# Kernel tuning notes

Hardware: AMD Instinct MI355X
Metric: run time of the kernel (lower is better)

## Reference

```python
import jax, jax.numpy as jnp
import numpy as np

B_SZ, T, C_DIM, N = 16, 2048, 128, 64
STEP = 0.01
LN_EPS = 1e-5


def _cplx(re, im):
    return (re + 1j * im).astype(jnp.complex64)


def s4_kernel(L_real, L_imag, P_real, P_imag, B_real, B_imag, C_real, C_imag, L):
    """DPLR generating-function kernel (annotated-S4 kernel_DPLR), vectorized over channels.
    Returns real kernel of shape (L, C)."""
    Lam = _cplx(jnp.minimum(L_real, 1e-4), L_imag)          # (C, N)
    P = _cplx(P_real, P_imag)                                # (C, N)
    Bm = _cplx(B_real, B_imag)                               # (C, N)
    Cm = _cplx(C_real, C_imag)                               # (C, N)
    Omega = jnp.exp(-2j * jnp.pi * jnp.arange(L) / L).astype(jnp.complex64)  # (L,)
    g = (2.0 / STEP) * ((1.0 - Omega) / (1.0 + Omega))       # (L,)
    c2 = 2.0 / (1.0 + Omega)                                 # (L,)

    def cauchy(v):  # v: (C, N) -> (L, C)
        return (v[None, :, :] / (g[:, None, None] - Lam[None, :, :])).sum(-1)

    k00 = cauchy(jnp.conj(Cm) * Bm)
    k01 = cauchy(jnp.conj(Cm) * P)
    k10 = cauchy(jnp.conj(P) * Bm)
    k11 = cauchy(jnp.conj(P) * P)
    at_roots = c2[:, None] * (k00 - k01 * (1.0 / (1.0 + k11)) * k10)  # (L, C)
    return jnp.fft.ifft(at_roots, n=L, axis=0).real          # (L, C)


def setup_inputs() -> dict:
    key = jax.random.key(0)
    ks = jax.random.split(key, 12)
    s = 1.0 / np.sqrt(N)
    return {
        "x": jax.random.normal(ks[0], (B_SZ, T, C_DIM), jnp.float32),
        "ln_gamma": jnp.ones((C_DIM,), jnp.float32),
        "ln_beta": jnp.zeros((C_DIM,), jnp.float32),
        "L_real": -0.5 * jnp.abs(jax.random.normal(ks[1], (C_DIM, N), jnp.float32)),
        "L_imag": jax.random.normal(ks[2], (C_DIM, N), jnp.float32) * float(np.pi),
        "P_real": jax.random.normal(ks[3], (C_DIM, N), jnp.float32) * s,
        "P_imag": jax.random.normal(ks[4], (C_DIM, N), jnp.float32) * s,
        "B_real": jax.random.normal(ks[5], (C_DIM, N), jnp.float32) * s,
        "B_imag": jax.random.normal(ks[6], (C_DIM, N), jnp.float32) * s,
        "C_real": jax.random.normal(ks[7], (C_DIM, N), jnp.float32) * float(np.sqrt(0.5)),
        "C_imag": jax.random.normal(ks[8], (C_DIM, N), jnp.float32) * float(np.sqrt(0.5)),
        "D": jnp.ones((C_DIM,), jnp.float32),
        "W_out": jax.random.normal(ks[9], (C_DIM, C_DIM), jnp.float32) / float(np.sqrt(C_DIM)),
        "b_out": jnp.zeros((C_DIM,), jnp.float32),
    }


def reference(x, ln_gamma, ln_beta, L_real, L_imag, P_real, P_imag,
              B_real, B_imag, C_real, C_imag, D, W_out, b_out):
    # pre-LayerNorm over channels
    mu = x.mean(-1, keepdims=True)
    var = ((x - mu) ** 2).mean(-1, keepdims=True)
    y = (x - mu) / jnp.sqrt(var + LN_EPS) * ln_gamma + ln_beta   # (B, T, C)

    # S4 FFT convolution (training path)
    kernel = s4_kernel(L_real, L_imag, P_real, P_imag,
                       B_real, B_imag, C_real, C_imag, T)       # (T, C)
    kf = jnp.fft.rfft(kernel, n=2 * T, axis=0)                  # (T+1, C)
    uf = jnp.fft.rfft(y, n=2 * T, axis=1)                        # (B, T+1, C)
    conv = jnp.fft.irfft(uf * kf[None], n=2 * T, axis=1)[:, :T, :]
    ssm_out = conv + D * y                                       # skip D*u

    # GELU (exact) -> Linear -> residual
    h = jax.nn.gelu(ssm_out, approximate=False)
    out = jnp.einsum("btc,oc->bto", h, W_out) + b_out
    return out + x
```

## Files before the change

kernel.cpp:

```cpp
#include <hip/hip_runtime.h>


#define PAD(i) ((i) + ((i) >> 4))

using bf16x8 = __attribute__((ext_vector_type(8))) short;
using f32x4 = __attribute__((ext_vector_type(4))) float;
typedef unsigned short ushort_t;

static __device__ __forceinline__ float2 cmulf(float2 a, float2 b) {
  return make_float2(a.x * b.x - a.y * b.y, a.x * b.y + a.y * b.x);
}
static __device__ __forceinline__ float2 cadd(float2 a, float2 b) { return make_float2(a.x + b.x, a.y + b.y); }
static __device__ __forceinline__ float2 csub(float2 a, float2 b) { return make_float2(a.x - b.x, a.y - b.y); }
static __device__ __forceinline__ float2 cconj(float2 a) { return make_float2(a.x, -a.y); }
static __device__ __forceinline__ float gelu1(float x) {
  float x2 = x * x;
  float z = x * fmaf(0.0356774081f, x2, 0.7978845608f);
  z = fminf(fmaxf(z, -15.0f), 15.0f);
  float e = __builtin_amdgcn_exp2f(z * 2.8853900817779268f);
  return x * e * __builtin_amdgcn_rcpf(e + 1.0f);
}
static __device__ __forceinline__ ushort_t f2bf(float f) {
  unsigned int u = __float_as_uint(f);
  u += 0x7FFFu + ((u >> 16) & 1u);
  return (ushort_t)(u >> 16);
}
static __device__ __forceinline__ float bf2f(ushort_t u) {
  return __uint_as_float(((unsigned int)u) << 16);
}
static __device__ __forceinline__ float2 twf(float rev) {
  return make_float2(__builtin_amdgcn_cosf(rev), -__builtin_amdgcn_sinf(rev));
}
static __device__ __forceinline__ float2 twi(float rev) {
  return make_float2(__builtin_amdgcn_cosf(rev), __builtin_amdgcn_sinf(rev));
}

template <bool INV>
static __device__ __forceinline__ void bf4g(float2& a, float2& b, float2& c, float2& d, float2 w1) {
  float2 t0 = cadd(a, c), t1 = csub(a, c), t2 = cadd(b, d), t3 = csub(b, d);
  float2 w2 = cmulf(w1, w1), w3 = cmulf(w2, w1);
  float2 o0 = cadd(t0, t2);
  float2 o1 = cmulf(csub(t0, t2), w2);
  float2 o2, o3;
  if (!INV) {
    o2 = cmulf(make_float2(t1.x + t3.y, t1.y - t3.x), w1);
    o3 = cmulf(make_float2(t1.x - t3.y, t1.y + t3.x), w3);
  } else {
    o2 = cmulf(make_float2(t1.x - t3.y, t1.y + t3.x), w1);
    o3 = cmulf(make_float2(t1.x + t3.y, t1.y - t3.x), w3);
  }
  a = o0; b = o1; c = o2; d = o3;
}
static __device__ __forceinline__ void bf4f(float2& a, float2& b, float2& c, float2& d, float2 w1) {
  bf4g<false>(a, b, c, d, w1);
}
static __device__ __forceinline__ void bf4f3(float2& a, float2& b, float2& c, float2& d,
                                             float2 w1, float2 w2, float2 w3) {
  float2 t0 = cadd(a, c), t1 = csub(a, c), t2 = cadd(b, d), t3 = csub(b, d);
  a = cadd(t0, t2);
  b = cmulf(csub(t0, t2), w2);
  c = cmulf(make_float2(t1.x + t3.y, t1.y - t3.x), w1);
  d = cmulf(make_float2(t1.x - t3.y, t1.y + t3.x), w3);
}
static __device__ __forceinline__ void bf4f1(float2& a, float2& b, float2& c, float2& d) {
  float2 t0 = cadd(a, c), t1 = csub(a, c), t2 = cadd(b, d), t3 = csub(b, d);
  a = cadd(t0, t2);
  b = csub(t0, t2);
  c = make_float2(t1.x + t3.y, t1.y - t3.x);
  d = make_float2(t1.x - t3.y, t1.y + t3.x);
}
static __device__ __forceinline__ void bf4f_z(float2 a, float2 b, float2 w1,
                                              float2& o0, float2& o1, float2& o2, float2& o3) {
  float2 w2 = cmulf(w1, w1), w3 = cmulf(w2, w1);
  o0 = cadd(a, b);
  o1 = cmulf(csub(a, b), w2);
  o2 = cmulf(make_float2(a.x + b.y, a.y - b.x), w1);
  o3 = cmulf(make_float2(a.x - b.y, a.y + b.x), w3);
}
template <bool INV>
static __device__ __forceinline__ void bf4h(float2& a, float2& b, float2& c, float2& d, float2 u1) {
  float2 u2 = cmulf(u1, u1);
  float2 tb = cmulf(b, u2), td = cmulf(d, u2);
  float2 a1 = cadd(a, tb), b1 = csub(a, tb), c1 = cadd(c, td), d1 = csub(c, td);
  float2 tc = cmulf(c1, u1), te = cmulf(d1, u1);
  a = cadd(a1, tc);
  c = csub(a1, tc);
  if (INV) {
    b = make_float2(b1.x - te.y, b1.y + te.x);
    d = make_float2(b1.x + te.y, b1.y - te.x);
  } else {
    b = make_float2(b1.x + te.y, b1.y - te.x);
    d = make_float2(b1.x - te.y, b1.y + te.x);
  }
}
static __device__ __forceinline__ void bf4i(float2& a, float2& b, float2& c, float2& d, float2 u1) {
  bf4h<true>(a, b, c, d, u1);
}
static __device__ __forceinline__ void bf4i3(float2& a, float2& b, float2& c, float2& d,
                                             float2 u1, float2 u2) {
  float2 tb = cmulf(b, u2), td = cmulf(d, u2);
  float2 a1 = cadd(a, tb), b1 = csub(a, tb), c1 = cadd(c, td), d1 = csub(c, td);
  float2 tc = cmulf(c1, u1), te = cmulf(d1, u1);
  a = cadd(a1, tc);
  c = csub(a1, tc);
  b = make_float2(b1.x - te.y, b1.y + te.x);
  d = make_float2(b1.x + te.y, b1.y - te.x);
}
static __device__ __forceinline__ void bf4i1(float2& a, float2& b, float2& c, float2& d) {
  float2 a1 = cadd(a, b), b1 = csub(a, b), c1 = cadd(c, d), d1 = csub(c, d);
  a = cadd(a1, c1);
  c = csub(a1, c1);
  b = make_float2(b1.x - d1.y, b1.y + d1.x);
  d = make_float2(b1.x + d1.y, b1.y - d1.x);
}

#define W256R 0.9238795325112867f
#define W256I -0.3826834323650898f
#define W512R 0.7071067811865476f
#define W512I -0.7071067811865476f
#define W768R 0.3826834323650898f
#define W768I -0.9238795325112867f

__global__ __launch_bounds__(256) void k_ln_ar(
    const float* __restrict__ x, const float* __restrict__ gamma, const float* __restrict__ beta,
    ushort_t* __restrict__ y_bf,
    const float* __restrict__ Lr, const float* __restrict__ Li,
    const float* __restrict__ Pr, const float* __restrict__ Pi,
    const float* __restrict__ Br, const float* __restrict__ Bi,
    const float* __restrict__ Cr, const float* __restrict__ Ci,
    float2* __restrict__ arr,
    const float* __restrict__ W, ushort_t* __restrict__ w_bf) {
  __shared__ __align__(16) char sm[17536];
  const int tid = threadIdx.x;
  if (blockIdx.x < 1024) {
    float* tile = (float*)sm;
    float* sg = (float*)(sm + 16512);
    float* sb = (float*)(sm + 17024);
    const int b = blockIdx.x >> 6;
    const int t0 = (blockIdx.x & 63) << 5;
    if (tid < 128) { sg[tid] = gamma[tid]; sb[tid] = beta[tid]; }
    const float4* __restrict__ xb4 = (const float4*)(x + ((size_t)b * 2048 + t0) * 128);
#pragma unroll
    for (int r = 0; r < 4; ++r) {
      int idx = tid + 256 * r;
      int t = idx >> 5, j = idx & 31;
      float4 v4 = xb4[idx];
      float* dst = &tile[t * 129 + 4 * j];
      dst[0] = v4.x; dst[1] = v4.y; dst[2] = v4.z; dst[3] = v4.w;
    }
    __syncthreads();
    const int row = tid >> 3, sgp = tid & 7;
    float sum = 0.f, sq = 0.f;
#pragma unroll
    for (int i = 0; i < 16; ++i) {
      float v = tile[row * 129 + sgp * 16 + i];
      sum += v;
      sq += v * v;
    }
    sum += __shfl_xor(sum, 1); sq += __shfl_xor(sq, 1);
    sum += __shfl_xor(sum, 2); sq += __shfl_xor(sq, 2);
    sum += __shfl_xor(sum, 4); sq += __shfl_xor(sq, 4);
    float mean = sum * (1.0f / 128.0f);
    float var = sq * (1.0f / 128.0f) - mean * mean;
    float rstd = 1.0f / sqrtf(var + 1e-5f);
#pragma unroll
    for (int i = 0; i < 16; ++i) {
      int cc = sgp * 16 + i;
      float v = tile[row * 129 + cc];
      tile[row * 129 + cc] = (v - mean) * rstd * sg[cc] + sb[cc];
    }
    __syncthreads();
    ushort_t* __restrict__ yb = y_bf + (size_t)b * 128 * 2048 + t0;
#pragma unroll
    for (int r = 0; r < 4; ++r) {
      int idx = tid + 256 * r;
      int cc = idx >> 3, tl4 = (idx & 7) * 4;
      ushort4 o4;
      o4.x = f2bf(tile[(tl4 + 0) * 129 + cc]);
      o4.y = f2bf(tile[(tl4 + 1) * 129 + cc]);
      o4.z = f2bf(tile[(tl4 + 2) * 129 + cc]);
      o4.w = f2bf(tile[(tl4 + 3) * 129 + cc]);
      *(ushort4*)(yb + (size_t)cc * 2048 + tl4) = o4;
    }
  } else if (blockIdx.x < 2048) {
    float2* sLam = (float2*)sm;
    float2* sv00 = sLam + 64;
    float2* sv01 = sLam + 128;
    float2* sv10 = sLam + 192;
    float2* sv11 = sLam + 256;
    const int id = blockIdx.x - 1024;
    const int c = id >> 3;
    const int l = ((id & 7) << 8) + tid;
    if (tid < 64) {
      int i = c * 64 + tid;
      float lr = fminf(Lr[i], 1e-4f), li = Li[i];
      float pr = Pr[i], pi = Pi[i];
      float br = Br[i], bi = Bi[i];
      float cr = Cr[i], ci = Ci[i];
      sLam[tid] = make_float2(lr, li);
      sv00[tid] = make_float2(cr * br + ci * bi, cr * bi - ci * br);
      sv01[tid] = make_float2(cr * pr + ci * pi, cr * pi - ci * pr);
      sv10[tid] = make_float2(pr * br + pi * bi, pr * bi - pi * br);
      sv11[tid] = make_float2(pr * pr + pi * pi, 0.0f);
    }
    __syncthreads();
    float theta = (-6.2831855f * (float)l) * (1.0f / 2048.0f);
    float om_i, om_r;
    sincosf(theta, &om_i, &om_r);
    float pr_ = 1.0f + om_r, pi_ = om_i;
    float mr_ = 1.0f - om_r, mi_ = -om_i;
    float invd = __builtin_amdgcn_rcpf(fmaf(pr_, pr_, pi_ * pi_));
    float gr = 200.0f * ((mr_ * pr_ + mi_ * pi_) * invd);
    float gi = 200.0f * ((mi_ * pr_ - mr_ * pi_) * invd);
    float c2r = 2.0f * pr_ * invd, c2i = -2.0f * pi_ * invd;
    float s00r = 0.f, s00i = 0.f, s01r = 0.f, s01i = 0.f;
    float s10r = 0.f, s10i = 0.f, s11r = 0.f, s11i = 0.f;
#pragma unroll 8
    for (int n = 0; n < 64; ++n) {
      float2 lam = sLam[n];
      float dr = gr - lam.x, di = gi - lam.y;
      float idn = __builtin_amdgcn_rcpf(fmaf(dr, dr, di * di));
      float ir = dr * idn, ii = -di * idn;
      float2 v;
      v = sv00[n]; s00r += v.x * ir - v.y * ii; s00i += v.x * ii + v.y * ir;
      v = sv01[n]; s01r += v.x * ir - v.y * ii; s01i += v.x * ii + v.y * ir;
      v = sv10[n]; s10r += v.x * ir - v.y * ii; s10i += v.x * ii + v.y * ir;
      v = sv11[n]; s11r += v.x * ir - v.y * ii; s11i += v.x * ii + v.y * ir;
    }
    float dr2 = 1.0f + s11r, di2 = s11i;
    float idn2 = __builtin_amdgcn_rcpf(fmaf(dr2, dr2, di2 * di2));
    float rr = dr2 * idn2, ri = -di2 * idn2;
    float t1r = s01r * rr - s01i * ri, t1i = s01r * ri + s01i * rr;
    float t2r = t1r * s10r - t1i * s10i, t2i = t1r * s10i + t1i * s10r;
    float fr = s00r - t2r, fi = s00i - t2i;
    arr[(size_t)c * 2048 + l] = make_float2(c2r * fr - c2i * fi, c2r * fi + c2i * fr);
  } else {
    const float4* __restrict__ W4 = (const float4*)W;
    ushort4* __restrict__ Wb4 = (ushort4*)w_bf;
#pragma unroll
    for (int m = 0; m < 16; ++m) {
      int idx = tid + 256 * m;
      float4 w4 = W4[idx];
      ushort4 u;
      u.x = f2bf(w4.x); u.y = f2bf(w4.y); u.z = f2bf(w4.z); u.w = f2bf(w4.w);
      Wb4[idx] = u;
    }
  }
}

template <int Q, bool INV>
static __device__ __forceinline__ void kfs_dif(float2* s, int tid) {
  constexpr float SCR = (float)(2048 / (4 * Q)) * (1.0f / 2048.0f);
  int k = tid;
  int j = k & (Q - 1);
  int i = ((k - j) << 2) + j;
  float2 w1 = INV ? twi((float)j * SCR) : twf((float)j * SCR);
  float2 a = s[PAD(i)], b = s[PAD(i + Q)], c2 = s[PAD(i + 2 * Q)], d = s[PAD(i + 3 * Q)];
  bf4g<INV>(a, b, c2, d, w1);
  s[PAD(i)] = a; s[PAD(i + Q)] = b; s[PAD(i + 2 * Q)] = c2; s[PAD(i + 3 * Q)] = d;
  __syncthreads();
}
template <int Q>
static __device__ __forceinline__ void kfs_dit(float2* s, int tid) {
  constexpr float SCR = (float)(2048 / (4 * Q)) * (1.0f / 2048.0f);
  int k = tid;
  int j = k & (Q - 1);
  int i = ((k - j) << 2) + j;
  float2 u1 = twf((float)j * SCR);
  float2 a = s[PAD(i)], b = s[PAD(i + Q)], c2 = s[PAD(i + 2 * Q)], d = s[PAD(i + 3 * Q)];
  bf4h<false>(a, b, c2, d, u1);
  s[PAD(i)] = a; s[PAD(i + Q)] = b; s[PAD(i + 2 * Q)] = c2; s[PAD(i + 3 * Q)] = d;
  __syncthreads();
}
static __device__ __forceinline__ void kfs_r2(float2* s, int tid) {
#pragma unroll
  for (int m = 0; m < 2; ++m) {
    int k = tid + 512 * m;
    int i = 2 * k;
    float2 a = s[PAD(i)], b = s[PAD(i + 1)];
    s[PAD(i)] = cadd(a, b);
    s[PAD(i + 1)] = csub(a, b);
  }
  __syncthreads();
}

__global__ __launch_bounds__(512) void k_kf(const float2* __restrict__ arr, float2* __restrict__ kf) {
  __shared__ float2 s[2176];
  const int tid = threadIdx.x;
  const int c = blockIdx.x;
  const float2* __restrict__ ac = arr + (size_t)c * 2048;
  float2* __restrict__ kfc = kf + (size_t)c * 4096;
#pragma unroll
  for (int m = 0; m < 4; ++m) {
    int q = tid + 512 * m;
    float2 aq = ac[q];
    s[PAD(q)] = aq;
    float2 am = ac[(2048 - q) & 2047];
    kfc[__brev((unsigned)q) >> 21] =
        make_float2((aq.x + am.x) * (0.5f / 4096.0f), (aq.y - am.y) * (0.5f / 4096.0f));
  }
  __syncthreads();
  kfs_dif<512, true>(s, tid);
  kfs_dif<128, true>(s, tid);
  kfs_dif<32, true>(s, tid);
  kfs_dif<8, true>(s, tid);
  kfs_dif<2, true>(s, tid);
  kfs_r2(s, tid);
#pragma unroll
  for (int m = 0; m < 4; ++m) {
    int p = tid + 512 * m;
    int t = (int)(__brev((unsigned)p) >> 21);
    float2 w = twf((float)t * (1.0f / 4096.0f));
    float kr = s[PAD(p)].x * (1.0f / 8388608.0f);
    s[PAD(p)] = make_float2(kr * w.x, kr * w.y);
  }
  __syncthreads();
  kfs_r2(s, tid);
  kfs_dit<2>(s, tid);
  kfs_dit<8>(s, tid);
  kfs_dit<32>(s, tid);
  kfs_dit<128>(s, tid);
  kfs_dit<512>(s, tid);
#pragma unroll
  for (int m = 0; m < 4; ++m) {
    int q = tid + 512 * m;
    kfc[2048 + (int)(__brev((unsigned)q) >> 21)] = s[PAD(q)];
  }
}

__global__ __launch_bounds__(256) void k_conv(const ushort_t* __restrict__ y_bf,
                                              const float2* __restrict__ kf,
                                              const float* __restrict__ D,
                                              ushort_t* __restrict__ h_bf) {
  __shared__ float2 s[4352];
  const int tid = threadIdx.x;
  const int p = blockIdx.x;
  const int b = p >> 7, c = p & 127;
  const ushort_t* __restrict__ r1 = y_bf + (size_t)(b * 128 + c) * 2048;
  const ushort_t* __restrict__ r2 = y_bf + (size_t)((b + 8) * 128 + c) * 2048;
  ushort_t* __restrict__ hb1 = h_bf + (size_t)(b * 128 + c) * 2048;
  ushort_t* __restrict__ hb2 = h_bf + (size_t)((b + 8) * 128 + c) * 2048;

  const float2 K1 = make_float2(W256R, W256I);
  const float2 K2 = make_float2(W512R, W512I);
  const float2 K3 = make_float2(W768R, W768I);

  float2 kreg[16];
  {
    const float2* __restrict__ kfc = kf + (size_t)c * 4096 + 16 * tid;
#pragma unroll
    for (int e = 0; e < 16; ++e) kreg[e] = kfc[e];
  }
  const float Dc = D[c];

  float2 v[16];
  {
    float2 ya[8];
#pragma unroll
    for (int e = 0; e < 8; ++e)
      ya[e] = make_float2(bf2f(r1[tid + 256 * e]), bf2f(r2[tid + 256 * e]));
    const float2 wt = twf((float)tid * (1.0f / 4096.0f));
    bf4f_z(ya[0], ya[4], wt,            v[0], v[4], v[8], v[12]);
    bf4f_z(ya[1], ya[5], cmulf(wt, K1), v[1], v[5], v[9], v[13]);
    bf4f_z(ya[2], ya[6], cmulf(wt, K2), v[2], v[6], v[10], v[14]);
    bf4f_z(ya[3], ya[7], cmulf(wt, K3), v[3], v[7], v[11], v[15]);
  }
  {
    const float2 wq = twf((float)tid * (1.0f / 1024.0f));
    const float2 wq2 = cmulf(wq, wq), wq3 = cmulf(wq2, wq);
    bf4f3(v[0], v[1], v[2], v[3], wq, wq2, wq3);
    bf4f3(v[4], v[5], v[6], v[7], wq, wq2, wq3);
    bf4f3(v[8], v[9], v[10], v[11], wq, wq2, wq3);
    bf4f3(v[12], v[13], v[14], v[15], wq, wq2, wq3);
  }
  {
    const int wb0 = tid + (tid >> 4);
#pragma unroll
    for (int e = 0; e < 16; ++e) s[272 * e + wb0] = v[e];
  }
  __syncthreads();
  const int a_ = tid >> 4, b_ = tid & 15;
  const int rbB = 272 * a_ + b_;
#pragma unroll
  for (int e = 0; e < 16; ++e) v[e] = s[rbB + 17 * e];
  {
    const float2 wb = twf((float)b_ * (1.0f / 256.0f));
    bf4f(v[0], v[4], v[8], v[12], wb);
    bf4f(v[1], v[5], v[9], v[13], cmulf(wb, K1));
    bf4f(v[2], v[6], v[10], v[14], cmulf(wb, K2));
    bf4f(v[3], v[7], v[11], v[15], cmulf(wb, K3));
  }
  {
    const float2 w16 = twf((float)b_ * (1.0f / 64.0f));
    const float2 w162 = cmulf(w16, w16), w163 = cmulf(w162, w16);
    bf4f3(v[0], v[1], v[2], v[3], w16, w162, w163);
    bf4f3(v[4], v[5], v[6], v[7], w16, w162, w163);
    bf4f3(v[8], v[9], v[10], v[11], w16, w162, w163);
    bf4f3(v[12], v[13], v[14], v[15], w16, w162, w163);
  }
#pragma unroll
  for (int e = 0; e < 16; ++e) s[rbB + 17 * e] = v[e];
  __syncthreads();
#pragma unroll
  for (int e = 0; e < 16; ++e) v[e] = s[17 * tid + e];
  __builtin_amdgcn_s_setprio(1);
  bf4f1(v[0], v[4], v[8], v[12]);
  bf4f(v[1], v[5], v[9], v[13], K1);
  bf4f(v[2], v[6], v[10], v[14], K2);
  bf4f(v[3], v[7], v[11], v[15], K3);
  bf4f1(v[0], v[1], v[2], v[3]);
  bf4f1(v[4], v[5], v[6], v[7]);
  bf4f1(v[8], v[9], v[10], v[11]);
  bf4f1(v[12], v[13], v[14], v[15]);
  {
    const float dsc = Dc * (1.0f / 4096.0f);
#pragma unroll
    for (int e = 0; e < 16; ++e) {
      float2 kv = kreg[e];
      kv.x += dsc;
      v[e] = cmulf(v[e], kv);
    }
  }
  bf4i1(v[0], v[1], v[2], v[3]);
  bf4i1(v[4], v[5], v[6], v[7]);
  bf4i1(v[8], v[9], v[10], v[11]);
  bf4i1(v[12], v[13], v[14], v[15]);
  bf4i1(v[0], v[4], v[8], v[12]);
  bf4i(v[1], v[5], v[9], v[13], cconj(K1));
  bf4i(v[2], v[6], v[10], v[14], cconj(K2));
  bf4i(v[3], v[7], v[11], v[15], cconj(K3));
  __builtin_amdgcn_s_setprio(0);
#pragma unroll
  for (int e = 0; e < 16; ++e) s[17 * tid + e] = v[e];
  __syncthreads();
#pragma unroll
  for (int e = 0; e < 16; ++e) v[e] = s[rbB + 17 * e];
  {
    const float2 w16c = twi((float)b_ * (1.0f / 64.0f));
    const float2 w16c2 = cmulf(w16c, w16c);
    bf4i3(v[0], v[1], v[2], v[3], w16c, w16c2);
    bf4i3(v[4], v[5], v[6], v[7], w16c, w16c2);
    bf4i3(v[8], v[9], v[10], v[11], w16c, w16c2);
    bf4i3(v[12], v[13], v[14], v[15], w16c, w16c2);
  }
  {
    const float2 wbc = twi((float)b_ * (1.0f / 256.0f));
    bf4i(v[0], v[4], v[8], v[12], wbc);
    bf4i(v[1], v[5], v[9], v[13], cmulf(wbc, cconj(K1)));
    bf4i(v[2], v[6], v[10], v[14], cmulf(wbc, cconj(K2)));
    bf4i(v[3], v[7], v[11], v[15], cmulf(wbc, cconj(K3)));
  }
#pragma unroll
  for (int e = 0; e < 16; ++e) s[rbB + 17 * e] = v[e];
  __syncthreads();
  {
    const int wb0 = tid + (tid >> 4);
#pragma unroll
    for (int e = 0; e < 16; ++e) v[e] = s[272 * e + wb0];
  }
  {
    const float2 wqc = twi((float)tid * (1.0f / 1024.0f));
    const float2 wqc2 = cmulf(wqc, wqc);
    bf4i3(v[0], v[1], v[2], v[3], wqc, wqc2);
    bf4i3(v[4], v[5], v[6], v[7], wqc, wqc2);
    bf4i3(v[8], v[9], v[10], v[11], wqc, wqc2);
    bf4i3(v[12], v[13], v[14], v[15], wqc, wqc2);
  }
  const float2 wtc = twi((float)tid * (1.0f / 4096.0f));
  auto fin = [&](float2 va, float2 vb, float2 vc2, float2 vd, float2 u1, int e0) {
    float2 u2 = cmulf(u1, u1);
    float2 tb = cmulf(vb, u2), td = cmulf(vd, u2);
    float2 a1 = cadd(va, tb), b1 = csub(va, tb), c1 = cadd(vc2, td), d1 = csub(vc2, td);
    float2 tc = cmulf(c1, u1), te = cmulf(d1, u1);
    float2 oa = cadd(a1, tc);
    float2 ob = make_float2(b1.x - te.y, b1.y + te.x);
    int i0 = tid + 256 * e0;
    hb1[i0] = f2bf(gelu1(oa.x));
    hb2[i0] = f2bf(gelu1(oa.y));
    hb1[i0 + 1024] = f2bf(gelu1(ob.x));
    hb2[i0 + 1024] = f2bf(gelu1(ob.y));
  };
  fin(v[0], v[4], v[8], v[12], wtc, 0);
  fin(v[1], v[5], v[9], v[13], cmulf(wtc, cconj(K1)), 1);
  fin(v[2], v[6], v[10], v[14], cmulf(wtc, cconj(K2)), 2);
  fin(v[3], v[7], v[11], v[15], cmulf(wtc, cconj(K3)), 3);
}

__global__ __launch_bounds__(256) void k_out(const ushort_t* __restrict__ h_bf,
                                             const ushort_t* __restrict__ w_bf,
                                             const float* __restrict__ bout,
                                             const float* __restrict__ x,
                                             float* __restrict__ out) {
  __shared__ __align__(16) char smem[52224];
  ushort_t* Wl = (ushort_t*)smem;
  ushort_t* hl = (ushort_t*)(smem + 34816);
  const int tid = threadIdx.x;
  const int b = blockIdx.x >> 5;
  const int t0 = (blockIdx.x & 31) << 6;

  {
    const ushort4* __restrict__ Wb4 = (const ushort4*)w_bf;
#pragma unroll
    for (int r = 0; r < 16; ++r) {
      int idx = tid + 256 * r;
      int o = idx >> 5, j = idx & 31;
      ushort4 u = Wb4[o * 32 + j];
      int sc = (((j >> 1) ^ (o & 15)) << 3) + 4 * (j & 1);
      *(ushort4*)&Wl[o * 136 + sc] = u;
    }
  }
  {
#pragma unroll
    for (int r = 0; r < 8; ++r) {
      int idx = tid + 256 * r;
      int cc = idx >> 4, t4 = (idx & 15) * 4;
      ushort4 hv = *(const ushort4*)&h_bf[((size_t)(b * 128 + cc)) * 2048 + t0 + t4];
      int cb = cc >> 3, clo = cc & 7;
#pragma unroll
      for (int i = 0; i < 4; ++i) {
        int t = t4 + i;
        hl[t * 136 + (((cb ^ (t & 15)) << 3) + clo)] = ((const ushort_t*)&hv)[i];
      }
    }
  }
  __syncthreads();

  const int l = tid & 63;
  const int w = tid >> 6;
  const int tl = l & 15;
  const int g = l >> 4;
  f32x4 acc[8];
#pragma unroll
  for (int i = 0; i < 8; ++i) acc[i] = (f32x4){0.f, 0.f, 0.f, 0.f};

#pragma unroll
  for (int ks = 0; ks < 4; ++ks) {
    int cb = ks * 4 + g;
    int col = ((cb ^ tl) << 3);
    bf16x8 bfrag = *(const bf16x8*)&hl[(16 * w + tl) * 136 + col];
#pragma unroll
    for (int ot = 0; ot < 8; ++ot) {
      bf16x8 afrag = *(const bf16x8*)&Wl[(ot * 16 + tl) * 136 + col];
      acc[ot] = __builtin_amdgcn_mfma_f32_16x16x32_bf16(afrag, bfrag, acc[ot], 0, 0, 0);
    }
  }
  const int t = t0 + 16 * w + tl;
  const size_t rowoff = ((size_t)b * 2048 + t) * 128;
#pragma unroll
  for (int ot = 0; ot < 8; ++ot) {
    int o = ot * 16 + g * 4;
    float4 xv = *(const float4*)&x[rowoff + o];
    float4 bo4 = *(const float4*)&bout[o];
    float4 v;
    v.x = acc[ot][0] + bo4.x + xv.x;
    v.y = acc[ot][1] + bo4.y + xv.y;
    v.z = acc[ot][2] + bo4.z + xv.z;
    v.w = acc[ot][3] + bo4.w + xv.w;
    *(float4*)&out[rowoff + o] = v;
  }
}


extern "C" void kernel_launch(void* const* d_in, const int* in_sizes, int n_in,
                              void* d_out, int out_size, void* d_ws, size_t ws_size,
                              hipStream_t stream) {
  (void)in_sizes; (void)n_in; (void)out_size; (void)ws_size;
  const float* x  = (const float*)d_in[0];
  const float* g  = (const float*)d_in[1];
  const float* be = (const float*)d_in[2];
  const float* Lr = (const float*)d_in[3];
  const float* Li = (const float*)d_in[4];
  const float* Pr = (const float*)d_in[5];
  const float* Pi = (const float*)d_in[6];
  const float* Br = (const float*)d_in[7];
  const float* Bi = (const float*)d_in[8];
  const float* Cr = (const float*)d_in[9];
  const float* Ci = (const float*)d_in[10];
  const float* D  = (const float*)d_in[11];
  const float* W  = (const float*)d_in[12];
  const float* bo = (const float*)d_in[13];
  float* out = (float*)d_out;

  char* ws = (char*)d_ws;
  ushort_t* y_bf = (ushort_t*)ws;
  float2*   arr  = (float2*)(ws + (16u << 20));
  float2*   kfb  = (float2*)(ws + (18u << 20));
  ushort_t* h_bf = (ushort_t*)(ws + (22u << 20));
  ushort_t* w_bf = (ushort_t*)(ws + (30u << 20));

  hipLaunchKernelGGL(k_ln_ar, dim3(2049), dim3(256), 0, stream,
                     x, g, be, y_bf, Lr, Li, Pr, Pi, Br, Bi, Cr, Ci, arr, W, w_bf);
  hipLaunchKernelGGL(k_kf,   dim3(128),  dim3(512), 0, stream, arr, kfb);
  hipLaunchKernelGGL(k_conv, dim3(1024), dim3(256), 0, stream, y_bf, kfb, D, h_bf);
  hipLaunchKernelGGL(k_out,  dim3(512),  dim3(256), 0, stream, h_bf, w_bf, bo, x, out);
}
```

Baseline: 66.31 us.

## Restructure conv FFT as radix-8 stages over 512 threads

```diff
diff --git a/kernel.cpp b/kernel.cpp
--- a/kernel.cpp
+++ b/kernel.cpp
@@ -2,6 +2,7 @@
 
 
 #define PAD(i) ((i) + ((i) >> 4))
+#define RSQ2 0.70710678118654752f
 
 using bf16x8 = __attribute__((ext_vector_type(8))) short;
 using f32x4 = __attribute__((ext_vector_type(4))) float;
@@ -50,32 +51,6 @@
     o3 = cmulf(make_float2(t1.x + t3.y, t1.y - t3.x), w3);
   }
   a = o0; b = o1; c = o2; d = o3;
-}
-static __device__ __forceinline__ void bf4f(float2& a, float2& b, float2& c, float2& d, float2 w1) {
-  bf4g<false>(a, b, c, d, w1);
-}
-static __device__ __forceinline__ void bf4f3(float2& a, float2& b, float2& c, float2& d,
-                                             float2 w1, float2 w2, float2 w3) {
-  float2 t0 = cadd(a, c), t1 = csub(a, c), t2 = cadd(b, d), t3 = csub(b, d);
-  a = cadd(t0, t2);
-  b = cmulf(csub(t0, t2), w2);
-  c = cmulf(make_float2(t1.x + t3.y, t1.y - t3.x), w1);
-  d = cmulf(make_float2(t1.x - t3.y, t1.y + t3.x), w3);
-}
-static __device__ __forceinline__ void bf4f1(float2& a, float2& b, float2& c, float2& d) {
-  float2 t0 = cadd(a, c), t1 = csub(a, c), t2 = cadd(b, d), t3 = csub(b, d);
-  a = cadd(t0, t2);
-  b = csub(t0, t2);
-  c = make_float2(t1.x + t3.y, t1.y - t3.x);
-  d = make_float2(t1.x - t3.y, t1.y + t3.x);
-}
-static __device__ __forceinline__ void bf4f_z(float2 a, float2 b, float2 w1,
-                                              float2& o0, float2& o1, float2& o2, float2& o3) {
-  float2 w2 = cmulf(w1, w1), w3 = cmulf(w2, w1);
-  o0 = cadd(a, b);
-  o1 = cmulf(csub(a, b), w2);
-  o2 = cmulf(make_float2(a.x + b.y, a.y - b.x), w1);
-  o3 = cmulf(make_float2(a.x - b.y, a.y + b.x), w3);
 }
 template <bool INV>
 static __device__ __forceinline__ void bf4h(float2& a, float2& b, float2& c, float2& d, float2 u1) {
@@ -93,33 +68,90 @@
     d = make_float2(b1.x - te.y, b1.y + te.x);
   }
 }
-static __device__ __forceinline__ void bf4i(float2& a, float2& b, float2& c, float2& d, float2 u1) {
-  bf4h<true>(a, b, c, d, u1);
-}
-static __device__ __forceinline__ void bf4i3(float2& a, float2& b, float2& c, float2& d,
-                                             float2 u1, float2 u2) {
-  float2 tb = cmulf(b, u2), td = cmulf(d, u2);
-  float2 a1 = cadd(a, tb), b1 = csub(a, tb), c1 = cadd(c, td), d1 = csub(c, td);
-  float2 tc = cmulf(c1, u1), te = cmulf(d1, u1);
-  a = cadd(a1, tc);
-  c = csub(a1, tc);
-  b = make_float2(b1.x - te.y, b1.y + te.x);
-  d = make_float2(b1.x + te.y, b1.y - te.x);
-}
-static __device__ __forceinline__ void bf4i1(float2& a, float2& b, float2& c, float2& d) {
-  float2 a1 = cadd(a, b), b1 = csub(a, b), c1 = cadd(c, d), d1 = csub(c, d);
-  a = cadd(a1, c1);
-  c = csub(a1, c1);
-  b = make_float2(b1.x - d1.y, b1.y + d1.x);
-  d = make_float2(b1.x + d1.y, b1.y - d1.x);
-}
-
-#define W256R 0.9238795325112867f
-#define W256I -0.3826834323650898f
-#define W512R 0.7071067811865476f
-#define W512I -0.7071067811865476f
-#define W768R 0.3826834323650898f
-#define W768I -0.9238795325112867f
+
+static __device__ __forceinline__ void r8f23(float2* v, float2 w2, float2 w3) {
+  float2 w2i = make_float2(w2.y, -w2.x);
+#pragma unroll
+  for (int q0 = 0; q0 < 8; q0 += 4) {
+    { float2 a = v[q0 + 0], b = v[q0 + 2]; v[q0 + 0] = cadd(a, b); v[q0 + 2] = cmulf(csub(a, b), w2); }
+    { float2 a = v[q0 + 1], b = v[q0 + 3]; v[q0 + 1] = cadd(a, b); v[q0 + 3] = cmulf(csub(a, b), w2i); }
+  }
+#pragma unroll
+  for (int e = 0; e < 8; e += 2) {
+    float2 a = v[e], b = v[e + 1];
+    v[e] = cadd(a, b);
+    v[e + 1] = cmulf(csub(a, b), w3);
+  }
+}
+static __device__ __forceinline__ void r8f(float2* v, float2 w1, float2 w2, float2 w3) {
+  float2 w1p1 = cmulf(w1, make_float2(RSQ2, -RSQ2));
+  float2 w1p2 = make_float2(w1.y, -w1.x);
+  float2 w1p3 = cmulf(w1, make_float2(-RSQ2, -RSQ2));
+  { float2 a = v[0], b = v[4]; v[0] = cadd(a, b); v[4] = cmulf(csub(a, b), w1); }
+  { float2 a = v[1], b = v[5]; v[1] = cadd(a, b); v[5] = cmulf(csub(a, b), w1p1); }
+  { float2 a = v[2], b = v[6]; v[2] = cadd(a, b); v[6] = cmulf(csub(a, b), w1p2); }
+  { float2 a = v[3], b = v[7]; v[3] = cadd(a, b); v[7] = cmulf(csub(a, b), w1p3); }
+  r8f23(v, w2, w3);
+}
+static __device__ __forceinline__ void r8f_const(float2* v) {
+  { float2 a = v[0], b = v[4]; v[0] = cadd(a, b); v[4] = csub(a, b); }
+  { float2 a = v[1], b = v[5]; float2 t = csub(a, b); v[1] = cadd(a, b);
+    v[5] = make_float2((t.x + t.y) * RSQ2, (t.y - t.x) * RSQ2); }
+  { float2 a = v[2], b = v[6]; float2 t = csub(a, b); v[2] = cadd(a, b);
+    v[6] = make_float2(t.y, -t.x); }
+  { float2 a = v[3], b = v[7]; float2 t = csub(a, b); v[3] = cadd(a, b);
+    v[7] = make_float2((t.y - t.x) * RSQ2, -(t.x + t.y) * RSQ2); }
+  { float2 a = v[0], b = v[2]; v[0] = cadd(a, b); v[2] = csub(a, b); }
+  { float2 a = v[1], b = v[3]; float2 t = csub(a, b); v[1] = cadd(a, b); v[3] = make_float2(t.y, -t.x); }
+  { float2 a = v[4], b = v[6]; v[4] = cadd(a, b); v[6] = csub(a, b); }
+  { float2 a = v[5], b = v[7]; float2 t = csub(a, b); v[5] = cadd(a, b); v[7] = make_float2(t.y, -t.x); }
+#pragma unroll
+  for (int e = 0; e < 8; e += 2) {
+    float2 a = v[e], b = v[e + 1];
+    v[e] = cadd(a, b);
+    v[e + 1] = csub(a, b);
+  }
+}
+static __device__ __forceinline__ void r8i(float2* v, float2 uA, float2 uB, float2 uC) {
+#pragma unroll
+  for (int e = 0; e < 8; e += 2) {
+    float2 t = cmulf(v[e + 1], uA);
+    float2 a = v[e];
+    v[e] = cadd(a, t);
+    v[e + 1] = csub(a, t);
+  }
+  float2 uBi = make_float2(-uB.y, uB.x);
+#pragma unroll
+  for (int q0 = 0; q0 < 8; q0 += 4) {
+    { float2 t = cmulf(v[q0 + 2], uB);  float2 a = v[q0 + 0]; v[q0 + 0] = cadd(a, t); v[q0 + 2] = csub(a, t); }
+    { float2 t = cmulf(v[q0 + 3], uBi); float2 a = v[q0 + 1]; v[q0 + 1] = cadd(a, t); v[q0 + 3] = csub(a, t); }
+  }
+  float2 uC1 = cmulf(uC, make_float2(RSQ2, RSQ2));
+  float2 uC2 = make_float2(-uC.y, uC.x);
+  float2 uC3 = cmulf(uC, make_float2(-RSQ2, RSQ2));
+  { float2 t = cmulf(v[4], uC);  float2 a = v[0]; v[0] = cadd(a, t); v[4] = csub(a, t); }
+  { float2 t = cmulf(v[5], uC1); float2 a = v[1]; v[1] = cadd(a, t); v[5] = csub(a, t); }
+  { float2 t = cmulf(v[6], uC2); float2 a = v[2]; v[2] = cadd(a, t); v[6] = csub(a, t); }
+  { float2 t = cmulf(v[7], uC3); float2 a = v[3]; v[3] = cadd(a, t); v[7] = csub(a, t); }
+}
+static __device__ __forceinline__ void r8i_const(float2* v) {
+#pragma unroll
+  for (int e = 0; e < 8; e += 2) {
+    float2 a = v[e], b = v[e + 1];
+    v[e] = cadd(a, b);
+    v[e + 1] = csub(a, b);
+  }
+  { float2 a = v[0], t = v[2]; v[0] = cadd(a, t); v[2] = csub(a, t); }
+  { float2 b = v[3]; float2 t = make_float2(-b.y, b.x); float2 a = v[1]; v[1] = cadd(a, t); v[3] = csub(a, t); }
+  { float2 a = v[4], t = v[6]; v[4] = cadd(a, t); v[6] = csub(a, t); }
+  { float2 b = v[7]; float2 t = make_float2(-b.y, b.x); float2 a = v[5]; v[5] = cadd(a, t); v[7] = csub(a, t); }
+  { float2 a = v[0], t = v[4]; v[0] = cadd(a, t); v[4] = csub(a, t); }
+  { float2 b = v[5]; float2 t = make_float2((b.x - b.y) * RSQ2, (b.x + b.y) * RSQ2);
+    float2 a = v[1]; v[1] = cadd(a, t); v[5] = csub(a, t); }
+  { float2 b = v[6]; float2 t = make_float2(-b.y, b.x); float2 a = v[2]; v[2] = cadd(a, t); v[6] = csub(a, t); }
+  { float2 b = v[7]; float2 t = make_float2(-(b.x + b.y) * RSQ2, (b.x - b.y) * RSQ2);
+    float2 a = v[3]; v[3] = cadd(a, t); v[7] = csub(a, t); }
+}
 
 __global__ __launch_bounds__(256) void k_ln_ar(
     const float* __restrict__ x, const float* __restrict__ gamma, const float* __restrict__ beta,
@@ -328,7 +360,7 @@
   }
 }
 
-__global__ __launch_bounds__(256) void k_conv(const ushort_t* __restrict__ y_bf,
+__global__ __launch_bounds__(512) void k_conv(const ushort_t* __restrict__ y_bf,
                                               const float2* __restrict__ kf,
                                               const float* __restrict__ D,
                                               ushort_t* __restrict__ h_bf) {
@@ -341,149 +373,107 @@
   ushort_t* __restrict__ hb1 = h_bf + (size_t)(b * 128 + c) * 2048;
   ushort_t* __restrict__ hb2 = h_bf + (size_t)((b + 8) * 128 + c) * 2048;
 
-  const float2 K1 = make_float2(W256R, W256I);
-  const float2 K2 = make_float2(W512R, W512I);
-  const float2 K3 = make_float2(W768R, W768I);
-
-  float2 kreg[16];
+  float2 kreg[8];
   {
-    const float2* __restrict__ kfc = kf + (size_t)c * 4096 + 16 * tid;
-#pragma unroll
-    for (int e = 0; e < 16; ++e) kreg[e] = kfc[e];
+    const float2* __restrict__ kfc = kf + (size_t)c * 4096 + 8 * tid;
+#pragma unroll
+    for (int e = 0; e < 8; ++e) kreg[e] = kfc[e];
   }
   const float Dc = D[c];
 
-  float2 v[16];
+  float2 v[8];
   {
-    float2 ya[8];
-#pragma unroll
-    for (int e = 0; e < 8; ++e)
-      ya[e] = make_float2(bf2f(r1[tid + 256 * e]), bf2f(r2[tid + 256 * e]));
-    const float2 wt = twf((float)tid * (1.0f / 4096.0f));
-    bf4f_z(ya[0], ya[4], wt,            v[0], v[4], v[8], v[12]);
-    bf4f_z(ya[1], ya[5], cmulf(wt, K1), v[1], v[5], v[9], v[13]);
-    bf4f_z(ya[2], ya[6], cmulf(wt, K2), v[2], v[6], v[10], v[14]);
-    bf4f_z(ya[3], ya[7], cmulf(wt, K3), v[3], v[7], v[11], v[15]);
-  }
-  {
-    const float2 wq = twf((float)tid * (1.0f / 1024.0f));
-    const float2 wq2 = cmulf(wq, wq), wq3 = cmulf(wq2, wq);
-    bf4f3(v[0], v[1], v[2], v[3], wq, wq2, wq3);
-    bf4f3(v[4], v[5], v[6], v[7], wq, wq2, wq3);
-    bf4f3(v[8], v[9], v[10], v[11], wq, wq2, wq3);
-    bf4f3(v[12], v[13], v[14], v[15], wq, wq2, wq3);
-  }
-  {
-    const int wb0 = tid + (tid >> 4);
-#pragma unroll
-    for (int e = 0; e < 16; ++e) s[272 * e + wb0] = v[e];
-  }
-  __syncthreads();
-  const int a_ = tid >> 4, b_ = tid & 15;
-  const int rbB = 272 * a_ + b_;
-#pragma unroll
-  for (int e = 0; e < 16; ++e) v[e] = s[rbB + 17 * e];
-  {
-    const float2 wb = twf((float)b_ * (1.0f / 256.0f));
-    bf4f(v[0], v[4], v[8], v[12], wb);
-    bf4f(v[1], v[5], v[9], v[13], cmulf(wb, K1));
-    bf4f(v[2], v[6], v[10], v[14], cmulf(wb, K2));
-    bf4f(v[3], v[7], v[11], v[15], cmulf(wb, K3));
-  }
-  {
-    const float2 w16 = twf((float)b_ * (1.0f / 64.0f));
-    const float2 w162 = cmulf(w16, w16), w163 = cmulf(w162, w16);
-    bf4f3(v[0], v[1], v[2], v[3], w16, w162, w163);
-    bf4f3(v[4], v[5], v[6], v[7], w16, w162, w163);
-    bf4f3(v[8], v[9], v[10], v[11], w16, w162, w163);
-    bf4f3(v[12], v[13], v[14], v[15], w16, w162, w163);
-  }
-#pragma unroll
-  for (int e = 0; e < 16; ++e) s[rbB + 17 * e] = v[e];
-  __syncthreads();
-#pragma unroll
-  for (int e = 0; e < 16; ++e) v[e] = s[17 * tid + e];
+#pragma unroll
+    for (int e = 0; e < 4; ++e) {
+      v[e] = make_float2(bf2f(r1[tid + 512 * e]), bf2f(r2[tid + 512 * e]));
+      v[e + 4] = make_float2(0.f, 0.f);
+    }
+    r8f(v, twf((float)tid * (1.0f / 4096.0f)), twf((float)tid * (1.0f / 2048.0f)),
+        twf((float)tid * (1.0f / 1024.0f)));
+  }
+#pragma unroll
+  for (int e = 0; e < 8; ++e) s[PAD(tid + 512 * e)] = v[e];
+  __syncthreads();
+  const int h = tid >> 6, l = tid & 63;
+#pragma unroll
+  for (int e = 0; e < 8; ++e) v[e] = s[PAD((h << 9) + (e << 6) + l)];
+  r8f(v, twf((float)l * (1.0f / 512.0f)), twf((float)l * (1.0f / 256.0f)),
+      twf((float)l * (1.0f / 128.0f)));
+#pragma unroll
+  for (int e = 0; e < 8; ++e) s[PAD((h << 9) + (e << 6) + l)] = v[e];
+  __syncthreads();
+  const int hh = tid >> 3, m = tid & 7;
+#pragma unroll
+  for (int e = 0; e < 8; ++e) v[e] = s[PAD((hh << 6) + (e << 3) + m)];
+  r8f(v, twf((float)m * (1.0f / 64.0f)), twf((float)m * (1.0f / 32.0f)),
+      twf((float)m * (1.0f / 16.0f)));
+#pragma unroll
+  for (int e = 0; e < 8; ++e) s[PAD((hh << 6) + (e << 3) + m)] = v[e];
+  __syncthreads();
+#pragma unroll
+  for (int e = 0; e < 8; ++e) v[e] = s[PAD(8 * tid + e)];
   __builtin_amdgcn_s_setprio(1);
-  bf4f1(v[0], v[4], v[8], v[12]);
-  bf4f(v[1], v[5], v[9], v[13], K1);
-  bf4f(v[2], v[6], v[10], v[14], K2);
-  bf4f(v[3], v[7], v[11], v[15], K3);
-  bf4f1(v[0], v[1], v[2], v[3]);
-  bf4f1(v[4], v[5], v[6], v[7]);
-  bf4f1(v[8], v[9], v[10], v[11]);
-  bf4f1(v[12], v[13], v[14], v[15]);
+  r8f_const(v);
   {
     const float dsc = Dc * (1.0f / 4096.0f);
 #pragma unroll
-    for (int e = 0; e < 16; ++e) {
+    for (int e = 0; e < 8; ++e) {
       float2 kv = kreg[e];
       kv.x += dsc;
       v[e] = cmulf(v[e], kv);
     }
   }
-  bf4i1(v[0], v[1], v[2], v[3]);
-  bf4i1(v[4], v[5], v[6], v[7]);
-  bf4i1(v[8], v[9], v[10], v[11]);
-  bf4i1(v[12], v[13], v[14], v[15]);
-  bf4i1(v[0], v[4], v[8], v[12]);
-  bf4i(v[1], v[5], v[9], v[13], cconj(K1));
-  bf4i(v[2], v[6], v[10], v[14], cconj(K2));
-  bf4i(v[3], v[7], v[11], v[15], cconj(K3));
+  r8i_const(v);
   __builtin_amdgcn_s_setprio(0);
 #pragma unroll
-  for (int e = 0; e < 16; ++e) s[17 * tid + e] = v[e];
-  __syncthreads();
-#pragma unroll
-  for (int e = 0; e < 16; ++e) v[e] = s[rbB + 17 * e];
+  for (int e = 0; e < 8; ++e) s[PAD(8 * tid + e)] = v[e];
+  __syncthreads();
+#pragma unroll
+  for (int e = 0; e < 8; ++e) v[e] = s[PAD((hh << 6) + (e << 3) + m)];
+  r8i(v, twi((float)m * (1.0f / 16.0f)), twi((float)m * (1.0f / 32.0f)),
+      twi((float)m * (1.0f / 64.0f)));
+#pragma unroll
+  for (int e = 0; e < 8; ++e) s[PAD((hh << 6) + (e << 3) + m)] = v[e];
+  __syncthreads();
+#pragma unroll
+  for (int e = 0; e < 8; ++e) v[e] = s[PAD((h << 9) + (e << 6) + l)];
+  r8i(v, twi((float)l * (1.0f / 128.0f)), twi((float)l * (1.0f / 256.0f)),
+      twi((float)l * (1.0f / 512.0f)));
+#pragma unroll
+  for (int e = 0; e < 8; ++e) s[PAD((h << 9) + (e << 6) + l)] = v[e];
+  __syncthreads();
+#pragma unroll
+  for (int e = 0; e < 8; ++e) v[e] = s[PAD(tid + 512 * e)];
   {
-    const float2 w16c = twi((float)b_ * (1.0f / 64.0f));
-    const float2 w16c2 = cmulf(w16c, w16c);
-    bf4i3(v[0], v[1], v[2], v[3], w16c, w16c2);
-    bf4i3(v[4], v[5], v[6], v[7], w16c, w16c2);
-    bf4i3(v[8], v[9], v[10], v[11], w16c, w16c2);
-    bf4i3(v[12], v[13], v[14], v[15], w16c, w16c2);
-  }
-  {
-    const float2 wbc = twi((float)b_ * (1.0f / 256.0f));
-    bf4i(v[0], v[4], v[8], v[12], wbc);
-    bf4i(v[1], v[5], v[9], v[13], cmulf(wbc, cconj(K1)));
-    bf4i(v[2], v[6], v[10], v[14], cmulf(wbc, cconj(K2)));
-    bf4i(v[3], v[7], v[11], v[15], cmulf(wbc, cconj(K3)));
-  }
-#pragma unroll
-  for (int e = 0; e < 16; ++e) s[rbB + 17 * e] = v[e];
-  __syncthreads();
-  {
-    const int wb0 = tid + (tid >> 4);
-#pragma unroll
-    for (int e = 0; e < 16; ++e) v[e] = s[272 * e + wb0];
-  }
-  {
-    const float2 wqc = twi((float)tid * (1.0f / 1024.0f));
-    const float2 wqc2 = cmulf(wqc, wqc);
-    bf4i3(v[0], v[1], v[2], v[3], wqc, wqc2);
-    bf4i3(v[4], v[5], v[6], v[7], wqc, wqc2);
-    bf4i3(v[8], v[9], v[10], v[11], wqc, wqc2);
-    bf4i3(v[12], v[13], v[14], v[15], wqc, wqc2);
-  }
-  const float2 wtc = twi((float)tid * (1.0f / 4096.0f));
-  auto fin = [&](float2 va, float2 vb, float2 vc2, float2 vd, float2 u1, int e0) {
-    float2 u2 = cmulf(u1, u1);
-    float2 tb = cmulf(vb, u2), td = cmulf(vd, u2);
-    float2 a1 = cadd(va, tb), b1 = csub(va, tb), c1 = cadd(vc2, td), d1 = csub(vc2, td);
-    float2 tc = cmulf(c1, u1), te = cmulf(d1, u1);
-    float2 oa = cadd(a1, tc);
-    float2 ob = make_float2(b1.x - te.y, b1.y + te.x);
-    int i0 = tid + 256 * e0;
-    hb1[i0] = f2bf(gelu1(oa.x));
-    hb2[i0] = f2bf(gelu1(oa.y));
-    hb1[i0 + 1024] = f2bf(gelu1(ob.x));
-    hb2[i0 + 1024] = f2bf(gelu1(ob.y));
-  };
-  fin(v[0], v[4], v[8], v[12], wtc, 0);
-  fin(v[1], v[5], v[9], v[13], cmulf(wtc, cconj(K1)), 1);
-  fin(v[2], v[6], v[10], v[14], cmulf(wtc, cconj(K2)), 2);
-  fin(v[3], v[7], v[11], v[15], cmulf(wtc, cconj(K3)), 3);
+    const float2 uA = twi((float)tid * (1.0f / 1024.0f));
+    const float2 uB = twi((float)tid * (1.0f / 2048.0f));
+    const float2 uC = twi((float)tid * (1.0f / 4096.0f));
+#pragma unroll
+    for (int e = 0; e < 8; e += 2) {
+      float2 t = cmulf(v[e + 1], uA);
+      float2 a = v[e];
+      v[e] = cadd(a, t);
+      v[e + 1] = csub(a, t);
+    }
+    float2 uBi = make_float2(-uB.y, uB.x);
+#pragma unroll
+    for (int q0 = 0; q0 < 8; q0 += 4) {
+      { float2 t = cmulf(v[q0 + 2], uB);  float2 a = v[q0 + 0]; v[q0 + 0] = cadd(a, t); v[q0 + 2] = csub(a, t); }
+      { float2 t = cmulf(v[q0 + 3], uBi); float2 a = v[q0 + 1]; v[q0 + 1] = cadd(a, t); v[q0 + 3] = csub(a, t); }
+    }
+    float2 uCp[4];
+    uCp[0] = uC;
+    uCp[1] = cmulf(uC, make_float2(RSQ2, RSQ2));
+    uCp[2] = make_float2(-uC.y, uC.x);
+    uCp[3] = cmulf(uC, make_float2(-RSQ2, RSQ2));
+#pragma unroll
+    for (int e = 0; e < 4; ++e) {
+      float2 oa = cadd(v[e], cmulf(v[e + 4], uCp[e]));
+      int i0 = tid + 512 * e;
+      hb1[i0] = f2bf(gelu1(oa.x));
+      hb2[i0] = f2bf(gelu1(oa.y));
+    }
+  }
 }
 
 __global__ __launch_bounds__(256) void k_out(const ushort_t* __restrict__ h_bf,
@@ -591,6 +581,6 @@
   hipLaunchKernelGGL(k_ln_ar, dim3(2049), dim3(256), 0, stream,
                      x, g, be, y_bf, Lr, Li, Pr, Pi, Br, Bi, Cr, Ci, arr, W, w_bf);
   hipLaunchKernelGGL(k_kf,   dim3(128),  dim3(512), 0, stream, arr, kfb);
-  hipLaunchKernelGGL(k_conv, dim3(1024), dim3(256), 0, stream, y_bf, kfb, D, h_bf);
+  hipLaunchKernelGGL(k_conv, dim3(1024), dim3(512), 0, stream, y_bf, kfb, D, h_bf);
   hipLaunchKernelGGL(k_out,  dim3(512),  dim3(256), 0, stream, h_bf, w_bf, bo, x, out);
 }
```

New measurement: 66.32 us. Within noise of the previous version (+0.0%).
